# Optimization experiments

Hardware: AMD Instinct MI355X
Metric: run time of the kernel (lower is better)

## Reference

```python
import jax, jax.numpy as jnp
import numpy as np

TAU = 0.07          # softmax temperature
THR = 0.3           # Jaccard similarity threshold for positive pairs
EPS_NORM = 1e-12    # F.normalize eps


def setup_inputs() -> dict:
    key = jax.random.key(0)
    k1, k2, k3 = jax.random.split(key, 3)
    N, D, A = 4096, 128, 512
    z1 = jax.random.normal(k1, (N, D), dtype=jnp.float32)
    z2 = jax.random.normal(k2, (N, D), dtype=jnp.float32)
    labels = jax.random.randint(k3, (N, A), 0, 2).astype(jnp.int32)
    return {"z1": z1, "z2": z2, "labels": labels}


def _l2_normalize(x):
    n = jnp.linalg.norm(x, axis=-1, keepdims=True)
    return x / jnp.maximum(n, EPS_NORM)


def reference(z1, z2, labels):
    # Implements the N > 1000 (chunked) branch of SupConLoss.forward,
    # vectorized over all anchors at once (chunking is just tiling; math identical).
    N = z1.shape[0]
    idx = jnp.arange(N)

    z1n = _l2_normalize(z1)                       # (N, D)
    z2n = _l2_normalize(z2)                       # (N, D)
    z_all = jnp.concatenate([z1n, z2n], axis=0)   # (2N, D)

    # Jaccard label similarity -> positive-pair mask
    lab = labels.astype(jnp.float32)              # (N, A)
    inter = lab @ lab.T                           # (N, N)
    s = lab.sum(axis=1, keepdims=True)            # (N, 1)
    union = s + s.T - inter
    jaccard = inter / (union + 1e-8)
    pos_label = jaccard >= THR                    # (N, N) bool

    # pos mask over 2N columns: label-positives in both halves,
    # augmented view [j, N+j] forced True, self column [j, j] forced False.
    pos_mask = jnp.concatenate([pos_label, pos_label], axis=1)  # (N, 2N)
    pos_mask = pos_mask.at[idx, N + idx].set(True)
    pos_mask = pos_mask.at[idx, idx].set(False)

    # similarity of z1 anchors against all 2N embeddings
    sim = (z1n @ z_all.T) / TAU                   # (N, 2N)
    sim = sim - jax.lax.stop_gradient(sim.max(axis=1, keepdims=True))
    exp_sim = jnp.exp(sim)

    # denominator excludes the self column [j, j]
    denom = exp_sim.sum(axis=1, keepdims=True) - exp_sim[idx, idx][:, None]
    log_prob = sim - jnp.log(denom + 1e-8)

    num_pos = jnp.maximum(pos_mask.sum(axis=1), 1)
    loss_per_sample = -jnp.where(pos_mask, log_prob, 0.0).sum(axis=1) / num_pos
    return loss_per_sample.sum() / N
```

## Files before the change

### kernel.cpp

```cpp
#include <hip/hip_runtime.h>
#include <math.h>

#define N_ROWS 4096
#define DIM    128
#define A_LAB  512
#define INV_TAU 14.285714285714286f
#define C_EXP   20.609929155556620f

typedef __attribute__((ext_vector_type(8))) short short8;
typedef __attribute__((ext_vector_type(4))) float f32x4;
typedef __attribute__((ext_vector_type(4))) int i32x4;
typedef __attribute__((ext_vector_type(16))) int i32x16;


__device__ __forceinline__ unsigned short f2bf(float f) {
  unsigned int u = __builtin_bit_cast(unsigned int, f);
  u += 0x7fffu + ((u >> 16) & 1u);
  return (unsigned short)(u >> 16);
}

__global__ __launch_bounds__(256) void k_norm_pack(
    const float* __restrict__ z1, const float* __restrict__ z2,
    const int* __restrict__ labels,
    unsigned int* __restrict__ zbf, uint2* __restrict__ labs8,
    int* __restrict__ s, float* __restrict__ part, float* __restrict__ out)
{
  {
    const int idx = blockIdx.x * 256 + threadIdx.x;
    if (idx < 3 * 4096) part[idx] = 0.0f;
    if (idx == 0) out[0] = 0.0f;
  }
  const int wave = threadIdx.x >> 6, lane = threadIdx.x & 63;
  const int r = blockIdx.x * 4 + wave;
  const float* src = (r < N_ROWS) ? (z1 + (size_t)r * DIM)
                                  : (z2 + (size_t)(r - N_ROWS) * DIM);
  float2 x = ((const float2*)src)[lane];
  float ss = x.x * x.x + x.y * x.y;
  #pragma unroll
  for (int off = 32; off > 0; off >>= 1) ss += __shfl_xor(ss, off);
  const float inv = 1.0f / fmaxf(sqrtf(ss), 1e-12f);
  const unsigned int lo = f2bf(x.x * inv);
  const unsigned int hi = f2bf(x.y * inv);
  {
    const int u = lane >> 2, p = lane & 3;
    const int kf = u >> 2, quad = u & 3;
    const int g = r >> 4;
    zbf[(size_t)(((g * 4 + kf) * 64) + ((r & 15) + (quad << 4))) * 4 + p] = (hi << 16) | lo;
  }

  if (r < N_ROWS) {
    const int4* lp = (const int4*)(labels + (size_t)r * A_LAB);
    const int4 a = lp[2 * lane], b = lp[2 * lane + 1];
    const unsigned int w0 = (unsigned int)(a.x != 0)       | ((unsigned int)(a.y != 0) << 8)
                          | ((unsigned int)(a.z != 0) << 16) | ((unsigned int)(a.w != 0) << 24);
    const unsigned int w1 = (unsigned int)(b.x != 0)       | ((unsigned int)(b.y != 0) << 8)
                          | ((unsigned int)(b.z != 0) << 16) | ((unsigned int)(b.w != 0) << 24);
    uint2 v; v.x = w0; v.y = w1;
    const int ul = lane >> 1, hp = lane & 1;
    const int ks = ul >> 1, h = ul & 1;
    const int g = r >> 5;
    labs8[(size_t)(((g * 16 + ks) * 64) + ((r & 31) + (h << 5))) * 2 + hp] = v;
    int cnt = __popc(w0) + __popc(w1);
    #pragma unroll
    for (int off = 32; off > 0; off >>= 1) cnt += __shfl_xor(cnt, off);
    if (lane == 0) s[r] = cnt;
  }
}

__global__ __launch_bounds__(256, 2) void k_fused(
    const unsigned char* __restrict__ labs8, const int* __restrict__ s,
    const unsigned short* __restrict__ zbf, float* __restrict__ part)
{
  __shared__ unsigned int pmL[128 * 4];
  const int tid = threadIdx.x;
  const int ibase = blockIdx.x * 128, jbase = blockIdx.y * 128;
  const int wave = tid >> 6, lane = tid & 63;
  const bool diag = (ibase == jbase);
  const char* gl = (const char*)labs8;
  const char* gz = (const char*)zbf;

  const int jwr = (wave >> 1) * 64, jwc = (wave & 1) * 64;
  const int col32 = lane & 31, h = lane >> 5;

  const int s3i = 3 * s[ibase + jwr + lane];
  const int s3j = 3 * s[jbase + jwc + lane];

  i32x16 jacc[2][2];
  #pragma unroll
  for (int rt = 0; rt < 2; ++rt)
    #pragma unroll
    for (int nt = 0; nt < 2; ++nt)
      #pragma unroll
      for (int e = 0; e < 16; ++e) jacc[rt][nt][e] = 0;

  const int gI = (ibase + jwr) >> 5;
  const int gJ = (jbase + jwc) >> 5;
  #pragma unroll
  for (int ks = 0; ks < 16; ++ks) {
    i32x4 a[2], b[2];
    #pragma unroll
    for (int rt = 0; rt < 2; ++rt)
      a[rt] = *(const i32x4*)(gl + (size_t)(((gI + rt) * 16 + ks) * 64 + lane) * 16);
    #pragma unroll
    for (int nt = 0; nt < 2; ++nt)
      b[nt] = *(const i32x4*)(gl + (size_t)(((gJ + nt) * 16 + ks) * 64 + lane) * 16);
    #pragma unroll
    for (int rt = 0; rt < 2; ++rt)
      #pragma unroll
      for (int nt = 0; nt < 2; ++nt)
        jacc[rt][nt] = __builtin_amdgcn_mfma_i32_32x32x32_i8(a[rt], b[nt], jacc[rt][nt], 0, 0, 0);
  }

  #pragma unroll
  for (int rt = 0; rt < 2; ++rt)
    #pragma unroll
    for (int nt = 0; nt < 2; ++nt) {
      const int wl = (jwc >> 5) + nt;
      const int sj = __shfl(s3j, nt * 32 + col32);
      #pragma unroll
      for (int reg = 0; reg < 16; ++reg) {
        const int r0 = (reg & 3) + 8 * (reg >> 2);
        const int si = __shfl(s3i, rt * 32 + r0 + 4 * h);
        const bool pred = 13 * jacc[rt][nt][reg] >= si + sj;
        const unsigned long long bal = __ballot(pred);
        const int lr = jwr + rt * 32 + r0;
        if (lane == 0)      pmL[lr * 4 + wl]       = (unsigned int)bal;
        else if (lane == 1) pmL[(lr + 4) * 4 + wl] = (unsigned int)(bal >> 32);
      }
    }

  const int col = lane & 15, quad = lane >> 4;
  const int swr = wave * 32;
  const int gA = (ibase + swr) >> 4;
  short8 afr[2][4];
  #pragma unroll
  for (int rt = 0; rt < 2; ++rt)
    #pragma unroll
    for (int kf = 0; kf < 4; ++kf)
      afr[rt][kf] = *(const short8*)(gz + (size_t)(((gA + rt) * 4 + kf) * 64 + lane) * 16);

  __syncthreads();

  uint4 pw[2][4];
  #pragma unroll
  for (int rt = 0; rt < 2; ++rt)
    #pragma unroll
    for (int reg = 0; reg < 4; ++reg)
      pw[rt][reg] = *(const uint4*)&pmL[(swr + rt * 16 + quad * 4 + reg) * 4];

  float lacc[2][4], Sacc[2][4], Pcnt[2][4];
  #pragma unroll
  for (int rt = 0; rt < 2; ++rt)
    #pragma unroll
    for (int reg = 0; reg < 4; ++reg) { lacc[rt][reg] = 0; Sacc[rt][reg] = 0; Pcnt[rt][reg] = 0; }

  #pragma unroll
  for (int half = 0; half < 2; ++half) {
    const int gB = ((half ? N_ROWS : 0) + jbase) >> 4;
    f32x4 acc[2][8];
    #pragma unroll
    for (int rt = 0; rt < 2; ++rt)
      #pragma unroll
      for (int nt = 0; nt < 8; ++nt) acc[rt][nt] = (f32x4){0, 0, 0, 0};

    #pragma unroll
    for (int nt = 0; nt < 8; ++nt) {
      short8 bfr[4];
      #pragma unroll
      for (int kf = 0; kf < 4; ++kf)
        bfr[kf] = *(const short8*)(gz + (size_t)(((gB + nt) * 4 + kf) * 64 + lane) * 16);
      #pragma unroll
      for (int rt = 0; rt < 2; ++rt)
        #pragma unroll
        for (int kf = 0; kf < 4; ++kf)
          acc[rt][nt] = __builtin_amdgcn_mfma_f32_16x16x32_bf16(
              afr[rt][kf], bfr[kf], acc[rt][nt], 0, 0, 0);
    }

    if (!diag) {
      #pragma unroll
      for (int rt = 0; rt < 2; ++rt)
        #pragma unroll
        for (int nt = 0; nt < 8; ++nt) {
          const int bitpos = (nt & 1) * 16 + col;
          #pragma unroll
          for (int reg = 0; reg < 4; ++reg) {
            const unsigned int w = ((const unsigned int*)&pw[rt][reg])[nt >> 1];
            const float d = acc[rt][nt][reg];
            lacc[rt][reg] += exp2f(fmaf(d, C_EXP, -C_EXP));
            if ((w >> bitpos) & 1) Sacc[rt][reg] += d;
          }
        }
    } else {
      const bool left = (half == 0);
      #pragma unroll
      for (int rt = 0; rt < 2; ++rt)
        #pragma unroll
        for (int nt = 0; nt < 8; ++nt) {
          const int joff = nt * 16 + col;
          const int jc = jbase + joff;
          const int bitpos = joff & 31;
          #pragma unroll
          for (int reg = 0; reg < 4; ++reg) {
            const int i = ibase + swr + rt * 16 + quad * 4 + reg;
            const unsigned int w = ((const unsigned int*)&pw[rt][reg])[nt >> 1];
            const float d = acc[rt][nt][reg];
            const bool bit = (w >> bitpos) & 1;
            const bool self = left && (jc == i);
            const bool pos = left ? (bit && !self) : (bit || (jc == i));
            const float e = exp2f(fmaf(d, C_EXP, -C_EXP));
            if (!self) lacc[rt][reg] += e;
            if (pos) { Sacc[rt][reg] += d; Pcnt[rt][reg] += 1.0f; }
          }
        }
    }
  }

  #pragma unroll
  for (int rt = 0; rt < 2; ++rt)
    #pragma unroll
    for (int reg = 0; reg < 4; ++reg) {
      float l = lacc[rt][reg], S = Sacc[rt][reg], P = Pcnt[rt][reg];
      #pragma unroll
      for (int m = 1; m < 16; m <<= 1) {
        l += __shfl_xor(l, m);
        S += __shfl_xor(S, m);
        if (diag) P += __shfl_xor(P, m);
      }
      if (col == 0) {
        const int i = ibase + swr + rt * 16 + quad * 4 + reg;
        if (!diag) {
          const uint4 w = pw[rt][reg];
          P = 2.0f * (float)(__popc(w.x) + __popc(w.y) + __popc(w.z) + __popc(w.w));
        }
        atomicAdd(&part[i], l);
        atomicAdd(&part[4096 + i], S);
        atomicAdd(&part[8192 + i], P);
      }
    }
}

__global__ __launch_bounds__(128) void k_loss(
    const float* __restrict__ part, float* __restrict__ out)
{
  const int a = blockIdx.x * 128 + threadIdx.x;
  const float l = part[a];
  const float S = part[4096 + a];
  const float P = part[8192 + a];
  const float np = fmaxf(P, 1.0f);
  float v = INV_TAU + logf(l + 1e-8f) - (S * INV_TAU) / np;
  #pragma unroll
  for (int off = 32; off > 0; off >>= 1) v += __shfl_xor(v, off);
  __shared__ float ws2[2];
  const int wave = threadIdx.x >> 6, lane = threadIdx.x & 63;
  if (lane == 0) ws2[wave] = v;
  __syncthreads();
  if (threadIdx.x == 0) atomicAdd(out, (ws2[0] + ws2[1]) * (1.0f / (float)N_ROWS));
}

extern "C" void kernel_launch(void* const* d_in, const int* in_sizes, int n_in,
                              void* d_out, int out_size, void* d_ws, size_t ws_size,
                              hipStream_t stream) {
  const float* z1 = (const float*)d_in[0];
  const float* z2 = (const float*)d_in[1];
  const int* labels = (const int*)d_in[2];
  float* out = (float*)d_out;
  char* ws = (char*)d_ws;

  unsigned int* zbf    = (unsigned int*)(ws);
  uint2* labs8         = (uint2*)(ws + 2097152);
  int* s               = (int*)(ws + 4194304);
  float* part          = (float*)(ws + 4210688);

  hipLaunchKernelGGL(k_norm_pack, dim3(2048), dim3(256), 0, stream,
                     z1, z2, labels, zbf, labs8, s, part, out);
  hipLaunchKernelGGL(k_fused, dim3(32, 32), dim3(256), 0, stream,
                     (const unsigned char*)labs8, s, (const unsigned short*)zbf, part);
  hipLaunchKernelGGL(k_loss, dim3(32), dim3(128), 0, stream, part, out);
}
```

Before: 114.0 us.

## Split fused tile work across 8 waves instead of 4

Doubles the threads per block in the fused Jaccard/similarity kernel to 512. Each wave now owns half as much of the 128x128 tile: one 32-column Jaccard slab and 16 similarity rows. The goal is fewer accumulator registers per wave and more resident waves to hide latency. The cost is that B fragments of z are loaded redundantly by more waves, each wave gets fewer MFMAs to reuse its loaded fragments, and atomics per row stay the same.

```diff
diff --git a/kernel.cpp b/kernel.cpp
--- a/kernel.cpp
+++ b/kernel.cpp
@@ -67,7 +67,7 @@
   }
 }
 
-__global__ __launch_bounds__(256, 2) void k_fused(
+__global__ __launch_bounds__(512, 4) void k_fused(
     const unsigned char* __restrict__ labs8, const int* __restrict__ s,
     const unsigned short* __restrict__ zbf, float* __restrict__ part)
 {
@@ -79,89 +79,72 @@
   const char* gl = (const char*)labs8;
   const char* gz = (const char*)zbf;
 
-  const int jwr = (wave >> 1) * 64, jwc = (wave & 1) * 64;
+  const int jwr = (wave >> 2) * 64;
+  const int jwc = (wave & 3) * 32;
   const int col32 = lane & 31, h = lane >> 5;
 
   const int s3i = 3 * s[ibase + jwr + lane];
-  const int s3j = 3 * s[jbase + jwc + lane];
-
-  i32x16 jacc[2][2];
+  const int s3j = 3 * s[jbase + jwc + col32];
+
+  i32x16 jacc[2];
   #pragma unroll
   for (int rt = 0; rt < 2; ++rt)
     #pragma unroll
-    for (int nt = 0; nt < 2; ++nt)
-      #pragma unroll
-      for (int e = 0; e < 16; ++e) jacc[rt][nt][e] = 0;
+    for (int e = 0; e < 16; ++e) jacc[rt][e] = 0;
 
   const int gI = (ibase + jwr) >> 5;
   const int gJ = (jbase + jwc) >> 5;
   #pragma unroll
   for (int ks = 0; ks < 16; ++ks) {
-    i32x4 a[2], b[2];
+    i32x4 a[2], b;
     #pragma unroll
     for (int rt = 0; rt < 2; ++rt)
       a[rt] = *(const i32x4*)(gl + (size_t)(((gI + rt) * 16 + ks) * 64 + lane) * 16);
-    #pragma unroll
-    for (int nt = 0; nt < 2; ++nt)
-      b[nt] = *(const i32x4*)(gl + (size_t)(((gJ + nt) * 16 + ks) * 64 + lane) * 16);
+    b = *(const i32x4*)(gl + (size_t)((gJ * 16 + ks) * 64 + lane) * 16);
     #pragma unroll
     for (int rt = 0; rt < 2; ++rt)
-      #pragma unroll
-      for (int nt = 0; nt < 2; ++nt)
-        jacc[rt][nt] = __builtin_amdgcn_mfma_i32_32x32x32_i8(a[rt], b[nt], jacc[rt][nt], 0, 0, 0);
-  }
-
+      jacc[rt] = __builtin_amdgcn_mfma_i32_32x32x32_i8(a[rt], b, jacc[rt], 0, 0, 0);
+  }
+
+  const int wl = wave & 3;
   #pragma unroll
   for (int rt = 0; rt < 2; ++rt)
     #pragma unroll
-    for (int nt = 0; nt < 2; ++nt) {
-      const int wl = (jwc >> 5) + nt;
-      const int sj = __shfl(s3j, nt * 32 + col32);
-      #pragma unroll
-      for (int reg = 0; reg < 16; ++reg) {
-        const int r0 = (reg & 3) + 8 * (reg >> 2);
-        const int si = __shfl(s3i, rt * 32 + r0 + 4 * h);
-        const bool pred = 13 * jacc[rt][nt][reg] >= si + sj;
-        const unsigned long long bal = __ballot(pred);
-        const int lr = jwr + rt * 32 + r0;
-        if (lane == 0)      pmL[lr * 4 + wl]       = (unsigned int)bal;
-        else if (lane == 1) pmL[(lr + 4) * 4 + wl] = (unsigned int)(bal >> 32);
-      }
+    for (int reg = 0; reg < 16; ++reg) {
+      const int r0 = (reg & 3) + 8 * (reg >> 2);
+      const int si = __shfl(s3i, rt * 32 + r0 + 4 * h);
+      const bool pred = 13 * jacc[rt][reg] >= si + s3j;
+      const unsigned long long bal = __ballot(pred);
+      const int lr = jwr + rt * 32 + r0;
+      if (lane == 0)      pmL[lr * 4 + wl]       = (unsigned int)bal;
+      else if (lane == 1) pmL[(lr + 4) * 4 + wl] = (unsigned int)(bal >> 32);
     }
 
   const int col = lane & 15, quad = lane >> 4;
-  const int swr = wave * 32;
-  const int gA = (ibase + swr) >> 4;
-  short8 afr[2][4];
-  #pragma unroll
-  for (int rt = 0; rt < 2; ++rt)
-    #pragma unroll
-    for (int kf = 0; kf < 4; ++kf)
-      afr[rt][kf] = *(const short8*)(gz + (size_t)(((gA + rt) * 4 + kf) * 64 + lane) * 16);
+  const int srow = wave * 16;
+  const int gA = (ibase + srow) >> 4;
+  short8 afr[4];
+  #pragma unroll
+  for (int kf = 0; kf < 4; ++kf)
+    afr[kf] = *(const short8*)(gz + (size_t)((gA * 4 + kf) * 64 + lane) * 16);
 
   __syncthreads();
 
-  uint4 pw[2][4];
-  #pragma unroll
-  for (int rt = 0; rt < 2; ++rt)
-    #pragma unroll
-    for (int reg = 0; reg < 4; ++reg)
-      pw[rt][reg] = *(const uint4*)&pmL[(swr + rt * 16 + quad * 4 + reg) * 4];
-
-  float lacc[2][4], Sacc[2][4], Pcnt[2][4];
-  #pragma unroll
-  for (int rt = 0; rt < 2; ++rt)
-    #pragma unroll
-    for (int reg = 0; reg < 4; ++reg) { lacc[rt][reg] = 0; Sacc[rt][reg] = 0; Pcnt[rt][reg] = 0; }
+  uint4 pw[4];
+  #pragma unroll
+  for (int reg = 0; reg < 4; ++reg)
+    pw[reg] = *(const uint4*)&pmL[(srow + quad * 4 + reg) * 4];
+
+  float lacc[4], Sacc[4], Pcnt[4];
+  #pragma unroll
+  for (int reg = 0; reg < 4; ++reg) { lacc[reg] = 0; Sacc[reg] = 0; Pcnt[reg] = 0; }
 
   #pragma unroll
   for (int half = 0; half < 2; ++half) {
     const int gB = ((half ? N_ROWS : 0) + jbase) >> 4;
-    f32x4 acc[2][8];
-    #pragma unroll
-    for (int rt = 0; rt < 2; ++rt)
-      #pragma unroll
-      for (int nt = 0; nt < 8; ++nt) acc[rt][nt] = (f32x4){0, 0, 0, 0};
+    f32x4 acc[8];
+    #pragma unroll
+    for (int nt = 0; nt < 8; ++nt) acc[nt] = (f32x4){0, 0, 0, 0};
 
     #pragma unroll
     for (int nt = 0; nt < 8; ++nt) {
@@ -170,74 +153,66 @@
       for (int kf = 0; kf < 4; ++kf)
         bfr[kf] = *(const short8*)(gz + (size_t)(((gB + nt) * 4 + kf) * 64 + lane) * 16);
       #pragma unroll
-      for (int rt = 0; rt < 2; ++rt)
+      for (int kf = 0; kf < 4; ++kf)
+        acc[nt] = __builtin_amdgcn_mfma_f32_16x16x32_bf16(afr[kf], bfr[kf], acc[nt], 0, 0, 0);
+    }
+
+    if (!diag) {
+      #pragma unroll
+      for (int nt = 0; nt < 8; ++nt) {
+        const int bitpos = (nt & 1) * 16 + col;
         #pragma unroll
-        for (int kf = 0; kf < 4; ++kf)
-          acc[rt][nt] = __builtin_amdgcn_mfma_f32_16x16x32_bf16(
-              afr[rt][kf], bfr[kf], acc[rt][nt], 0, 0, 0);
-    }
-
-    if (!diag) {
-      #pragma unroll
-      for (int rt = 0; rt < 2; ++rt)
-        #pragma unroll
-        for (int nt = 0; nt < 8; ++nt) {
-          const int bitpos = (nt & 1) * 16 + col;
-          #pragma unroll
-          for (int reg = 0; reg < 4; ++reg) {
-            const unsigned int w = ((const unsigned int*)&pw[rt][reg])[nt >> 1];
-            const float d = acc[rt][nt][reg];
-            lacc[rt][reg] += exp2f(fmaf(d, C_EXP, -C_EXP));
-            if ((w >> bitpos) & 1) Sacc[rt][reg] += d;
-          }
+        for (int reg = 0; reg < 4; ++reg) {
+          const unsigned int w = ((const unsigned int*)&pw[reg])[nt >> 1];
+          const float d = acc[nt][reg];
+          lacc[reg] += exp2f(fmaf(d, C_EXP, -C_EXP));
+          if ((w >> bitpos) & 1) Sacc[reg] += d;
         }
+      }
     } else {
       const bool left = (half == 0);
       #pragma unroll
-      for (int rt = 0; rt < 2; ++rt)
+      for (int nt = 0; nt < 8; ++nt) {
+        const int joff = nt * 16 + col;
+        const int jc = jbase + joff;
+        const int bitpos = joff & 31;
         #pragma unroll
-        for (int nt = 0; nt < 8; ++nt) {
-          const int joff = nt * 16 + col;
-          const int jc = jbase + joff;
-          const int bitpos = joff & 31;
-          #pragma unroll
-          for (int reg = 0; reg < 4; ++reg) {
-            const int i = ibase + swr + rt * 16 + quad * 4 + reg;
-            const unsigned int w = ((const unsigned int*)&pw[rt][reg])[nt >> 1];
-            const float d = acc[rt][nt][reg];
-            const bool bit = (w >> bitpos) & 1;
-            const bool self = left && (jc == i);
-            const bool pos = left ? (bit && !self) : (bit || (jc == i));
-            const float e = exp2f(fmaf(d, C_EXP, -C_EXP));
-            if (!self) lacc[rt][reg] += e;
-            if (pos) { Sacc[rt][reg] += d; Pcnt[rt][reg] += 1.0f; }
-          }
+        for (int reg = 0; reg < 4; ++reg) {
+          const int i = ibase + srow + quad * 4 + reg;
+          const unsigned int w = ((const unsigned int*)&pw[reg])[nt >> 1];
+          const float d = acc[nt][reg];
+          const bool bit = (w >> bitpos) & 1;
+          const bool self = left && (jc == i);
+          const bool pos = left ? (bit && !self) : (bit || (jc == i));
+          const float e = exp2f(fmaf(d, C_EXP, -C_EXP));
+          if (!self) lacc[reg] += e;
+          if (pos) { Sacc[reg] += d; Pcnt[reg] += 1.0f; }
         }
-    }
-  }
-
-  #pragma unroll
-  for (int rt = 0; rt < 2; ++rt)
-    #pragma unroll
-    for (int reg = 0; reg < 4; ++reg) {
-      float l = lacc[rt][reg], S = Sacc[rt][reg], P = Pcnt[rt][reg];
-      #pragma unroll
-      for (int m = 1; m < 16; m <<= 1) {
-        l += __shfl_xor(l, m);
-        S += __shfl_xor(S, m);
-        if (diag) P += __shfl_xor(P, m);
       }
-      if (col == 0) {
-        const int i = ibase + swr + rt * 16 + quad * 4 + reg;
-        if (!diag) {
-          const uint4 w = pw[rt][reg];
-          P = 2.0f * (float)(__popc(w.x) + __popc(w.y) + __popc(w.z) + __popc(w.w));
-        }
-        atomicAdd(&part[i], l);
-        atomicAdd(&part[4096 + i], S);
-        atomicAdd(&part[8192 + i], P);
+    }
+  }
+
+  #pragma unroll
+  for (int reg = 0; reg < 4; ++reg) {
+    float l = lacc[reg], S = Sacc[reg], P = Pcnt[reg];
+    #pragma unroll
+    for (int m = 1; m < 16; m <<= 1) {
+      l += __shfl_xor(l, m);
+      S += __shfl_xor(S, m);
+      if (diag) P += __shfl_xor(P, m);
+    }
+    if (col == 0) {
+      const int li = srow + quad * 4 + reg;
+      const int i = ibase + li;
+      if (!diag) {
+        const uint4 w = pw[reg];
+        P = 2.0f * (float)(__popc(w.x) + __popc(w.y) + __popc(w.z) + __popc(w.w));
       }
-    }
+      atomicAdd(&part[i], l);
+      atomicAdd(&part[4096 + i], S);
+      atomicAdd(&part[8192 + i], P);
+    }
+  }
 }
 
 __global__ __launch_bounds__(128) void k_loss(
@@ -274,7 +249,7 @@
 
   hipLaunchKernelGGL(k_norm_pack, dim3(2048), dim3(256), 0, stream,
                      z1, z2, labels, zbf, labs8, s, part, out);
-  hipLaunchKernelGGL(k_fused, dim3(32, 32), dim3(256), 0, stream,
+  hipLaunchKernelGGL(k_fused, dim3(32, 32), dim3(512), 0, stream,
                      (const unsigned char*)labs8, s, (const unsigned short*)zbf, part);
   hipLaunchKernelGGL(k_loss, dim3(32), dim3(128), 0, stream, part, out);
 }
```

After: 107.8 us. 1.06x faster.

## Retile similarity GEMM to 2x2 wave grid of 64x64 tiles, raise occupancy

Applied to the files above, without the earlier changes.

Each wave now computes a 64x64 sub-tile of the similarity matrix over a 2x2 wave grid, instead of a 32x128 strip with preloaded A fragments. A and B fragments are loaded per k-step, which cuts the global load volume per MFMA. Each wave reads only its two mask words per row, and the non-diagonal positive count uses those two words. Launch bounds raise the block-per-CU hint to 3, which may cap registers tightly enough to cause spills given the 4x4 accumulators.

```diff
diff --git a/kernel.cpp b/kernel.cpp
--- a/kernel.cpp
+++ b/kernel.cpp
@@ -67,7 +67,7 @@
   }
 }
 
-__global__ __launch_bounds__(256, 2) void k_fused(
+__global__ __launch_bounds__(256, 3) void k_fused(
     const unsigned char* __restrict__ labs8, const int* __restrict__ s,
     const unsigned short* __restrict__ zbf, float* __restrict__ part)
 {
@@ -75,11 +75,12 @@
   const int tid = threadIdx.x;
   const int ibase = blockIdx.x * 128, jbase = blockIdx.y * 128;
   const int wave = tid >> 6, lane = tid & 63;
+  const int wr = wave >> 1, wc = wave & 1;
   const bool diag = (ibase == jbase);
   const char* gl = (const char*)labs8;
   const char* gz = (const char*)zbf;
 
-  const int jwr = (wave >> 1) * 64, jwc = (wave & 1) * 64;
+  const int jwr = wr * 64, jwc = wc * 64;
   const int col32 = lane & 31, h = lane >> 5;
 
   const int s3i = 3 * s[ibase + jwr + lane];
@@ -115,7 +116,7 @@
   for (int rt = 0; rt < 2; ++rt)
     #pragma unroll
     for (int nt = 0; nt < 2; ++nt) {
-      const int wl = (jwc >> 5) + nt;
+      const int wl = wc * 2 + nt;
       const int sj = __shfl(s3j, nt * 32 + col32);
       #pragma unroll
       for (int reg = 0; reg < 16; ++reg) {
@@ -129,63 +130,59 @@
       }
     }
 
+  __syncthreads();
+
   const int col = lane & 15, quad = lane >> 4;
-  const int swr = wave * 32;
+  const int swr = wr * 64, swc = wc * 64;
   const int gA = (ibase + swr) >> 4;
-  short8 afr[2][4];
-  #pragma unroll
-  for (int rt = 0; rt < 2; ++rt)
-    #pragma unroll
-    for (int kf = 0; kf < 4; ++kf)
-      afr[rt][kf] = *(const short8*)(gz + (size_t)(((gA + rt) * 4 + kf) * 64 + lane) * 16);
-
-  __syncthreads();
-
-  uint4 pw[2][4];
-  #pragma unroll
-  for (int rt = 0; rt < 2; ++rt)
+
+  uint2 pw[4][4];
+  #pragma unroll
+  for (int rt = 0; rt < 4; ++rt)
     #pragma unroll
     for (int reg = 0; reg < 4; ++reg)
-      pw[rt][reg] = *(const uint4*)&pmL[(swr + rt * 16 + quad * 4 + reg) * 4];
-
-  float lacc[2][4], Sacc[2][4], Pcnt[2][4];
-  #pragma unroll
-  for (int rt = 0; rt < 2; ++rt)
+      pw[rt][reg] = *(const uint2*)&pmL[(swr + rt * 16 + quad * 4 + reg) * 4 + wc * 2];
+
+  float lacc[4][4], Sacc[4][4], Pcnt[4][4];
+  #pragma unroll
+  for (int rt = 0; rt < 4; ++rt)
     #pragma unroll
     for (int reg = 0; reg < 4; ++reg) { lacc[rt][reg] = 0; Sacc[rt][reg] = 0; Pcnt[rt][reg] = 0; }
 
   #pragma unroll
   for (int half = 0; half < 2; ++half) {
-    const int gB = ((half ? N_ROWS : 0) + jbase) >> 4;
-    f32x4 acc[2][8];
-    #pragma unroll
-    for (int rt = 0; rt < 2; ++rt)
-      #pragma unroll
-      for (int nt = 0; nt < 8; ++nt) acc[rt][nt] = (f32x4){0, 0, 0, 0};
-
-    #pragma unroll
-    for (int nt = 0; nt < 8; ++nt) {
-      short8 bfr[4];
-      #pragma unroll
-      for (int kf = 0; kf < 4; ++kf)
-        bfr[kf] = *(const short8*)(gz + (size_t)(((gB + nt) * 4 + kf) * 64 + lane) * 16);
-      #pragma unroll
-      for (int rt = 0; rt < 2; ++rt)
+    const int gB = (((half ? N_ROWS : 0) + jbase + swc) >> 4);
+    f32x4 acc[4][4];
+    #pragma unroll
+    for (int rt = 0; rt < 4; ++rt)
+      #pragma unroll
+      for (int nt = 0; nt < 4; ++nt) acc[rt][nt] = (f32x4){0, 0, 0, 0};
+
+    #pragma unroll
+    for (int kf = 0; kf < 4; ++kf) {
+      short8 a[4], b[4];
+      #pragma unroll
+      for (int rt = 0; rt < 4; ++rt)
+        a[rt] = *(const short8*)(gz + (size_t)(((gA + rt) * 4 + kf) * 64 + lane) * 16);
+      #pragma unroll
+      for (int nt = 0; nt < 4; ++nt)
+        b[nt] = *(const short8*)(gz + (size_t)(((gB + nt) * 4 + kf) * 64 + lane) * 16);
+      #pragma unroll
+      for (int rt = 0; rt < 4; ++rt)
         #pragma unroll
-        for (int kf = 0; kf < 4; ++kf)
-          acc[rt][nt] = __builtin_amdgcn_mfma_f32_16x16x32_bf16(
-              afr[rt][kf], bfr[kf], acc[rt][nt], 0, 0, 0);
+        for (int nt = 0; nt < 4; ++nt)
+          acc[rt][nt] = __builtin_amdgcn_mfma_f32_16x16x32_bf16(a[rt], b[nt], acc[rt][nt], 0, 0, 0);
     }
 
     if (!diag) {
       #pragma unroll
-      for (int rt = 0; rt < 2; ++rt)
+      for (int rt = 0; rt < 4; ++rt)
         #pragma unroll
-        for (int nt = 0; nt < 8; ++nt) {
+        for (int nt = 0; nt < 4; ++nt) {
           const int bitpos = (nt & 1) * 16 + col;
           #pragma unroll
           for (int reg = 0; reg < 4; ++reg) {
-            const unsigned int w = ((const unsigned int*)&pw[rt][reg])[nt >> 1];
+            const unsigned int w = (nt >> 1) ? pw[rt][reg].y : pw[rt][reg].x;
             const float d = acc[rt][nt][reg];
             lacc[rt][reg] += exp2f(fmaf(d, C_EXP, -C_EXP));
             if ((w >> bitpos) & 1) Sacc[rt][reg] += d;
@@ -194,16 +191,16 @@
     } else {
       const bool left = (half == 0);
       #pragma unroll
-      for (int rt = 0; rt < 2; ++rt)
+      for (int rt = 0; rt < 4; ++rt)
         #pragma unroll
-        for (int nt = 0; nt < 8; ++nt) {
-          const int joff = nt * 16 + col;
+        for (int nt = 0; nt < 4; ++nt) {
+          const int joff = swc + nt * 16 + col;
           const int jc = jbase + joff;
           const int bitpos = joff & 31;
           #pragma unroll
           for (int reg = 0; reg < 4; ++reg) {
             const int i = ibase + swr + rt * 16 + quad * 4 + reg;
-            const unsigned int w = ((const unsigned int*)&pw[rt][reg])[nt >> 1];
+            const unsigned int w = (nt >> 1) ? pw[rt][reg].y : pw[rt][reg].x;
             const float d = acc[rt][nt][reg];
             const bool bit = (w >> bitpos) & 1;
             const bool self = left && (jc == i);
@@ -217,7 +214,7 @@
   }
 
   #pragma unroll
-  for (int rt = 0; rt < 2; ++rt)
+  for (int rt = 0; rt < 4; ++rt)
     #pragma unroll
     for (int reg = 0; reg < 4; ++reg) {
       float l = lacc[rt][reg], S = Sacc[rt][reg], P = Pcnt[rt][reg];
@@ -230,8 +227,8 @@
       if (col == 0) {
         const int i = ibase + swr + rt * 16 + quad * 4 + reg;
         if (!diag) {
-          const uint4 w = pw[rt][reg];
-          P = 2.0f * (float)(__popc(w.x) + __popc(w.y) + __popc(w.z) + __popc(w.w));
+          const uint2 w = pw[rt][reg];
+          P = 2.0f * (float)(__popc(w.x) + __popc(w.y));
         }
         atomicAdd(&part[i], l);
         atomicAdd(&part[4096 + i], S);
```

Measured after the change: 135.2 us. 1.19x slower.
